# Kernel optimization log

Hardware: AMD Instinct MI355X
Metric: run time of the kernel (lower is better)

## Reference

```python
import jax, jax.numpy as jnp
import numpy as np

# dims
B = 4096; BEGIN = 0; END = 2048; N_OBJ = 64; D_OBJ = 32
PI_IN = 31; PI_H = 256; EMB = 256; H = 4; HD = 64; OTH_IN = 256; OTH_H = 256; OTH_OUT = 256

def _lin_init(k, fan_in, fan_out):
    b = np.sqrt(6.0 / (fan_in + fan_out))
    return jax.random.uniform(k, (fan_in, fan_out), jnp.float32, -b, b)

def setup_inputs() -> dict:
    key = jax.random.key(0)
    ks = jax.random.split(key, 8)
    obs = jax.random.normal(ks[0], (B, BEGIN + (END - BEGIN) + OTH_IN), jnp.float32)
    inp = {
        "obs": obs,
        # others encoder MLP: 256 -> 256 -> 256
        "oW1": _lin_init(ks[1], OTH_IN, OTH_H), "ob1": jnp.zeros((OTH_H,), jnp.float32),
        "oW2": _lin_init(ks[2], OTH_H, OTH_OUT), "ob2": jnp.zeros((OTH_OUT,), jnp.float32),
        # per-object pi MLP: 31 -> 256 -> 256 -> 256
        "pW1": _lin_init(ks[3], PI_IN, PI_H), "pb1": jnp.zeros((PI_H,), jnp.float32),
        "pW2": _lin_init(ks[4], PI_H, PI_H), "pb2": jnp.zeros((PI_H,), jnp.float32),
        "pW3": _lin_init(ks[5], PI_H, EMB), "pb3": jnp.zeros((EMB,), jnp.float32),
        # attention projections
        "Wq": _lin_init(ks[6], OTH_OUT, H * HD), "bq": jnp.zeros((H * HD,), jnp.float32),
        # per-head K/V projections (MultiHeadProj): [H, HD, HD], stored as x @ W per head
        "Wk": jax.random.uniform(jax.random.fold_in(key, 10), (H, HD, HD), jnp.float32, -np.sqrt(6.0/(2*HD)), np.sqrt(6.0/(2*HD))),
        "bk": jnp.zeros((H, HD), jnp.float32),
        "Wv": jax.random.uniform(jax.random.fold_in(key, 11), (H, HD, HD), jnp.float32, -np.sqrt(6.0/(2*HD)), np.sqrt(6.0/(2*HD))),
        "bv": jnp.zeros((H, HD), jnp.float32),
    }
    return inp

def reference(obs, oW1, ob1, oW2, ob2, pW1, pb1, pW2, pb2, pW3, pb3, Wq, bq, Wk, bk, Wv, bv):
    # split obs
    objs = obs[:, BEGIN:END].reshape(-1, N_OBJ, D_OBJ)
    others = jnp.concatenate([obs[:, :BEGIN], obs[:, END:]], axis=1)
    # others encoder
    others_e = jax.nn.relu(others @ oW1 + ob1) @ oW2 + ob2           # [B, 256]
    # mask + per-object MLP
    mask = objs[:, :, -1]                                            # [B, N]
    feats = objs[:, :, :-1]                                          # [B, N, 31]
    h = jax.nn.relu(feats @ pW1 + pb1)
    h = jax.nn.relu(h @ pW2 + pb2)
    emb = (h @ pW3 + pb3) * mask[:, :, None]                         # [B, N, EMB]
    # attention
    q = (others_e @ Wq + bq).reshape(-1, H, 1, HD)                   # [B, H, 1, HD]
    e = emb.reshape(-1, N_OBJ, H, HD)                                # [B, N, H, HD]
    key = jnp.einsum('bnhd,hde->bnhe', e, Wk) + bk                   # per-head linear
    val = (jnp.einsum('bnhd,hde->bnhe', e, Wv) + bv) * mask[:, :, None, None]
    logits = jnp.einsum('bhqd,bnhd->bhqn', q, key) / np.sqrt(EMB)    # [B, H, 1, N]
    logits = jnp.where(mask[:, None, None, :] == 0, -1e9, logits)
    attn = jax.nn.softmax(logits, axis=-1)
    out_emb = jnp.einsum('bhqn,bnhd->bhqd', attn, val).reshape(-1, EMB)
    return jnp.concatenate([others_e, out_emb], axis=1)             # [B, 512]
```

## Files before the change

kernel.cpp:

```cpp
#include <hip/hip_runtime.h>

#define BATCH      4096
#define OBS_COLS   2304
#define OTH_OFF    2048
#define EMB        256
#define OUTC       512

#define QK_BYTES   (4096u * 256u * 4u)
#define QB_BYTES   (4096u * 4u * 4u)

typedef __bf16 bf16x8 __attribute__((ext_vector_type(8)));
typedef __bf16 bf16x4 __attribute__((ext_vector_type(4)));
typedef float  f32x16 __attribute__((ext_vector_type(16)));

#define S_PW1  0
#define S_PW2  2
#define S_PW3  18
#define N_SLICE 34

__device__ __forceinline__ int shx(int row, int col) {
    return (row << 8) + ((((col >> 3) ^ (row & 31)) << 3) | (col & 7));
}

__global__ __launch_bounds__(512, 2) void k_oth(
    const float* __restrict__ obs,
    const float* __restrict__ oW1, const float* __restrict__ ob1,
    const float* __restrict__ oW2, const float* __restrict__ ob2,
    const float* __restrict__ Wq,  const float* __restrict__ bq,
    const float* __restrict__ Wk,  const float* __restrict__ bk,
    const float* __restrict__ pW1, const float* __restrict__ pW2,
    const float* __restrict__ pW3,
    float* __restrict__ out, float* __restrict__ qkg,
    float* __restrict__ qbg, __bf16* __restrict__ wp)
{
    __shared__ __align__(16) __bf16 s_a[32 * 256];
    __shared__ __align__(16) __bf16 s_h[32 * 256];
    __shared__ __align__(16) __bf16 s_q[32 * 256];
    __shared__ float s_qb[32 * 4];

    const int t  = threadIdx.x;
    const int b0 = blockIdx.x * 32;
    const int wv = t >> 6, lane = t & 63;
    const int lm = lane & 31, lh = lane >> 5;
    const int ct = wv;

    if (blockIdx.x < N_SLICE) {
        const int s = blockIdx.x;
        int kt; const float* W; int isW1 = 0;
        if      (s < S_PW2) { kt = s;         W = pW1; isW1 = 1; }
        else if (s < S_PW3) { kt = s - S_PW2; W = pW2; }
        else                { kt = s - S_PW3; W = pW3; }
        const int kbase = kt * 16 + lh * 8;
        const int n     = (t >> 6) * 32 + lm;
        bf16x8 v;
        #pragma unroll
        for (int j = 0; j < 8; ++j) {
            const int k = kbase + j;
            const float f = (isW1 && k >= 31) ? 0.0f : W[k * 256 + n];
            v[j] = (__bf16)f;
        }
        ((bf16x8*)wp)[(size_t)s * 512 + t] = v;
    }

    #pragma unroll
    for (int i = 0; i < 2; ++i) {
        const int c = i * 512 + t;
        const int row = c >> 5, seg = c & 31;
        const float* src = obs + (size_t)(b0 + row) * OBS_COLS + OTH_OFF + seg * 8;
        const float4 v0 = ((const float4*)src)[0];
        const float4 v1 = ((const float4*)src)[1];
        bf16x8 o;
        o[0]=(__bf16)v0.x; o[1]=(__bf16)v0.y; o[2]=(__bf16)v0.z; o[3]=(__bf16)v0.w;
        o[4]=(__bf16)v1.x; o[5]=(__bf16)v1.y; o[6]=(__bf16)v1.z; o[7]=(__bf16)v1.w;
        *(bf16x8*)&s_a[shx(row, seg * 8)] = o;
    }
    if (t < 128) s_qb[t] = 0.0f;
    __syncthreads();

    f32x16 acc;
    f32x16 vzero;
    #pragma unroll
    for (int i = 0; i < 16; ++i) vzero[i] = 0.0f;

    {
        const float* Wl = oW1 + (size_t)(lh * 8) * 256 + ct * 32 + lm;
        acc = vzero;
        float f[8];
        #pragma unroll
        for (int j = 0; j < 8; ++j) f[j] = Wl[j * 256];
        #pragma unroll 4
        for (int kt = 0; kt < 16; ++kt) {
            float fn[8];
            const int kn = (kt + 1) & 15;
            #pragma unroll
            for (int j = 0; j < 8; ++j) fn[j] = Wl[(kn * 16 + j) * 256];
            bf16x8 b;
            #pragma unroll
            for (int j = 0; j < 8; ++j) b[j] = (__bf16)f[j];
            const bf16x8 a = *(const bf16x8*)&s_a[shx(lm, kt * 16 + lh * 8)];
            acc = __builtin_amdgcn_mfma_f32_32x32x16_bf16(b, a, acc, 0, 0, 0);
            #pragma unroll
            for (int j = 0; j < 8; ++j) f[j] = fn[j];
        }
        const float* bias = &ob1[ct * 32 + 4 * lh];
        #pragma unroll
        for (int g = 0; g < 4; ++g) {
            bf16x4 v;
            #pragma unroll
            for (int q = 0; q < 4; ++q)
                v[q] = (__bf16)fmaxf(acc[g * 4 + q] + bias[8 * g + q], 0.0f);
            *(bf16x4*)&s_h[(lm << 8) + ((((ct << 2) + g) ^ lm) << 3) + 4 * lh] = v;
        }
    }
    __syncthreads();

    {
        const float* Wl = oW2 + (size_t)(lh * 8) * 256 + ct * 32 + lm;
        acc = vzero;
        float f[8];
        #pragma unroll
        for (int j = 0; j < 8; ++j) f[j] = Wl[j * 256];
        #pragma unroll 4
        for (int kt = 0; kt < 16; ++kt) {
            float fn[8];
            const int kn = (kt + 1) & 15;
            #pragma unroll
            for (int j = 0; j < 8; ++j) fn[j] = Wl[(kn * 16 + j) * 256];
            bf16x8 b;
            #pragma unroll
            for (int j = 0; j < 8; ++j) b[j] = (__bf16)f[j];
            const bf16x8 a = *(const bf16x8*)&s_h[shx(lm, kt * 16 + lh * 8)];
            acc = __builtin_amdgcn_mfma_f32_32x32x16_bf16(b, a, acc, 0, 0, 0);
            #pragma unroll
            for (int j = 0; j < 8; ++j) f[j] = fn[j];
        }
        const float* bias = &ob2[ct * 32 + 4 * lh];
        float* dstg = &out[(size_t)(b0 + lm) * OUTC + ct * 32 + 4 * lh];
        #pragma unroll
        for (int g = 0; g < 4; ++g) {
            float4 fv; bf16x4 v;
            float* fp = &fv.x;
            #pragma unroll
            for (int q = 0; q < 4; ++q) {
                const float f2 = acc[g * 4 + q] + bias[8 * g + q];
                fp[q] = f2; v[q] = (__bf16)f2;
            }
            *(float4*)&dstg[8 * g] = fv;
            *(bf16x4*)&s_a[(lm << 8) + ((((ct << 2) + g) ^ lm) << 3) + 4 * lh] = v;
        }
    }
    __syncthreads();

    {
        const float* Wl = Wq + (size_t)(lh * 8) * 256 + ct * 32 + lm;
        acc = vzero;
        float f[8];
        #pragma unroll
        for (int j = 0; j < 8; ++j) f[j] = Wl[j * 256];
        #pragma unroll 4
        for (int kt = 0; kt < 16; ++kt) {
            float fn[8];
            const int kn = (kt + 1) & 15;
            #pragma unroll
            for (int j = 0; j < 8; ++j) fn[j] = Wl[(kn * 16 + j) * 256];
            bf16x8 b;
            #pragma unroll
            for (int j = 0; j < 8; ++j) b[j] = (__bf16)f[j];
            const bf16x8 a = *(const bf16x8*)&s_a[shx(lm, kt * 16 + lh * 8)];
            acc = __builtin_amdgcn_mfma_f32_32x32x16_bf16(b, a, acc, 0, 0, 0);
            #pragma unroll
            for (int j = 0; j < 8; ++j) f[j] = fn[j];
        }
        const int hh = ct >> 1;
        const float* bias = &bq[ct * 32 + 4 * lh];
        const float* bkp  = &bk[ct * 32 + 4 * lh];
        float part = 0.0f;
        #pragma unroll
        for (int g = 0; g < 4; ++g) {
            bf16x4 v;
            #pragma unroll
            for (int q = 0; q < 4; ++q) {
                const float f2 = acc[g * 4 + q] + bias[8 * g + q];
                part += f2 * bkp[8 * g + q];
                v[q] = (__bf16)f2;
            }
            *(bf16x4*)&s_q[(lm << 8) + ((((ct << 2) + g) ^ lm) << 3) + 4 * lh] = v;
        }
        part += __shfl_xor(part, 32, 64);
        if (lane < 32) atomicAdd(&s_qb[lm * 4 + hh], part);
    }
    __syncthreads();

    if (t < 128) qbg[(size_t)(b0 + (t >> 2)) * 4 + (t & 3)] = s_qb[t];

    {
        const int h = wv >> 1, c2 = wv & 1;
        acc = vzero;
        #pragma unroll
        for (int kt = 0; kt < 4; ++kt) {
            const float* wk = Wk + ((size_t)(h * 64 + c2 * 32 + lm) * 64 + kt * 16 + lh * 8);
            const float4 w0 = *(const float4*)wk;
            const float4 w1 = *(const float4*)(wk + 4);
            bf16x8 b;
            b[0]=(__bf16)w0.x; b[1]=(__bf16)w0.y; b[2]=(__bf16)w0.z; b[3]=(__bf16)w0.w;
            b[4]=(__bf16)w1.x; b[5]=(__bf16)w1.y; b[6]=(__bf16)w1.z; b[7]=(__bf16)w1.w;
            const bf16x8 a = *(const bf16x8*)&s_q[shx(lm, h * 64 + kt * 16 + lh * 8)];
            acc = __builtin_amdgcn_mfma_f32_32x32x16_bf16(b, a, acc, 0, 0, 0);
        }
        float* dstg = &qkg[(size_t)(b0 + lm) * 256 + h * 64 + c2 * 32 + 4 * lh];
        #pragma unroll
        for (int g = 0; g < 4; ++g) {
            float4 fv;
            float* fp = &fv.x;
            #pragma unroll
            for (int q = 0; q < 4; ++q) fp[q] = acc[g * 4 + q];
            *(float4*)&dstg[8 * g] = fv;
        }
    }
}

__global__ __launch_bounds__(256, 4) void k_obj(
    const float* __restrict__ obs,  const __bf16* __restrict__ wp,
    const float* __restrict__ pb1,  const float* __restrict__ pb2,
    const float* __restrict__ pb3,  const float* __restrict__ qkg,
    const float* __restrict__ qbg,  const float* __restrict__ bv,
    const float* __restrict__ Wv,   float* __restrict__ out)
{
    __shared__ __align__(16) __bf16 s_h[64 * 256];
    __shared__ __align__(16) char s_fp[64 * 32 * 2];
    __bf16* s_f = (__bf16*)s_fp;
    float*  s_p = (float*)s_fp;
    __shared__ float s_mask[64];
    __shared__ float s_qk[4 * 64];
    __shared__ float s_am[4 * 64];
    __shared__ float s_amsum[4];
    __shared__ float s_qb[4];

    const int t  = threadIdx.x;
    const int b  = blockIdx.x;
    const int wv = t >> 6, lane = t & 63;
    const int lm = lane & 31, lh = lane >> 5;
    const int ct0 = wv * 2;
    const int row0 = lm;
    const int row1 = lm + 32;

    bf16x8 b1[2][2];
    {
        const bf16x8* Bg = (const bf16x8*)wp + S_PW1 * 512;
        #pragma unroll
        for (int kt = 0; kt < 2; ++kt)
            #pragma unroll
            for (int c = 0; c < 2; ++c)
                b1[kt][c] = Bg[(kt * 8 + ct0 + c) * 64 + lane];
    }

    {
        const int row = t >> 2, q4 = t & 3;
        const float* src = obs + (size_t)b * OBS_COLS + row * 32 + q4 * 8;
        const float4 v0 = ((const float4*)src)[0];
        const float4 v1 = ((const float4*)src)[1];
        bf16x8 o;
        o[0]=(__bf16)v0.x; o[1]=(__bf16)v0.y; o[2]=(__bf16)v0.z; o[3]=(__bf16)v0.w;
        o[4]=(__bf16)v1.x; o[5]=(__bf16)v1.y; o[6]=(__bf16)v1.z; o[7]=(__bf16)v1.w;
        *(bf16x8*)&s_f[row * 32 + q4 * 8] = o;
        if (q4 == 3) s_mask[row] = v1.w;
    }
    if (t < 64) ((float4*)s_qk)[t] = ((const float4*)(qkg + (size_t)b * 256))[t];
    if (t >= 64 && t < 68) s_qb[t - 64] = qbg[(size_t)b * 4 + (t - 64)];
    __syncthreads();

    f32x16 acc[2][2];
    f32x16 vzero;
    #pragma unroll
    for (int i = 0; i < 16; ++i) vzero[i] = 0.0f;

    {
        #pragma unroll
        for (int r = 0; r < 2; ++r)
            #pragma unroll
            for (int c = 0; c < 2; ++c) acc[r][c] = vzero;
        #pragma unroll
        for (int kt = 0; kt < 2; ++kt) {
            const bf16x8 a0 = *(const bf16x8*)&s_f[row0 * 32 + kt * 16 + lh * 8];
            const bf16x8 a1 = *(const bf16x8*)&s_f[row1 * 32 + kt * 16 + lh * 8];
            acc[0][0] = __builtin_amdgcn_mfma_f32_32x32x16_bf16(b1[kt][0], a0, acc[0][0], 0, 0, 0);
            acc[0][1] = __builtin_amdgcn_mfma_f32_32x32x16_bf16(b1[kt][1], a0, acc[0][1], 0, 0, 0);
            acc[1][0] = __builtin_amdgcn_mfma_f32_32x32x16_bf16(b1[kt][0], a1, acc[1][0], 0, 0, 0);
            acc[1][1] = __builtin_amdgcn_mfma_f32_32x32x16_bf16(b1[kt][1], a1, acc[1][1], 0, 0, 0);
        }
        #pragma unroll
        for (int r = 0; r < 2; ++r) {
            const int row = r ? row1 : row0;
            #pragma unroll
            for (int c = 0; c < 2; ++c) {
                const float* bias = &pb1[(ct0 + c) * 32 + 4 * lh];
                #pragma unroll
                for (int g = 0; g < 4; ++g) {
                    bf16x4 v;
                    #pragma unroll
                    for (int q = 0; q < 4; ++q)
                        v[q] = (__bf16)fmaxf(acc[r][c][g * 4 + q] + bias[8 * g + q], 0.0f);
                    *(bf16x4*)&s_h[(row << 8) + (((((ct0 + c) << 2) + g) ^ lm) << 3) + 4 * lh] = v;
                }
            }
        }
    }
    __syncthreads();

    {
        const bf16x8* Bg = (const bf16x8*)wp + S_PW2 * 512;
        #pragma unroll
        for (int r = 0; r < 2; ++r)
            #pragma unroll
            for (int c = 0; c < 2; ++c) acc[r][c] = vzero;
        bf16x8 bc0 = Bg[(ct0 + 0) * 64 + lane];
        bf16x8 bc1 = Bg[(ct0 + 1) * 64 + lane];
        #pragma unroll 4
        for (int kt = 0; kt < 16; ++kt) {
            const int kn = (kt + 1) & 15;
            const bf16x8 bn0 = Bg[(kn * 8 + ct0 + 0) * 64 + lane];
            const bf16x8 bn1 = Bg[(kn * 8 + ct0 + 1) * 64 + lane];
            const bf16x8 a0 = *(const bf16x8*)&s_h[(row0 << 8) + (((2 * kt + lh) ^ lm) << 3)];
            const bf16x8 a1 = *(const bf16x8*)&s_h[(row1 << 8) + (((2 * kt + lh) ^ lm) << 3)];
            acc[0][0] = __builtin_amdgcn_mfma_f32_32x32x16_bf16(bc0, a0, acc[0][0], 0, 0, 0);
            acc[0][1] = __builtin_amdgcn_mfma_f32_32x32x16_bf16(bc1, a0, acc[0][1], 0, 0, 0);
            acc[1][0] = __builtin_amdgcn_mfma_f32_32x32x16_bf16(bc0, a1, acc[1][0], 0, 0, 0);
            acc[1][1] = __builtin_amdgcn_mfma_f32_32x32x16_bf16(bc1, a1, acc[1][1], 0, 0, 0);
            bc0 = bn0; bc1 = bn1;
        }
        __syncthreads();
        #pragma unroll
        for (int r = 0; r < 2; ++r) {
            const int row = r ? row1 : row0;
            #pragma unroll
            for (int c = 0; c < 2; ++c) {
                const float* bias = &pb2[(ct0 + c) * 32 + 4 * lh];
                #pragma unroll
                for (int g = 0; g < 4; ++g) {
                    bf16x4 v;
                    #pragma unroll
                    for (int q = 0; q < 4; ++q)
                        v[q] = (__bf16)fmaxf(acc[r][c][g * 4 + q] + bias[8 * g + q], 0.0f);
                    *(bf16x4*)&s_h[(row << 8) + (((((ct0 + c) << 2) + g) ^ lm) << 3) + 4 * lh] = v;
                }
            }
        }
    }
    __syncthreads();

    {
        const bf16x8* Bg = (const bf16x8*)wp + S_PW3 * 512;
        #pragma unroll
        for (int r = 0; r < 2; ++r)
            #pragma unroll
            for (int c = 0; c < 2; ++c) acc[r][c] = vzero;
        bf16x8 bc0 = Bg[(ct0 + 0) * 64 + lane];
        bf16x8 bc1 = Bg[(ct0 + 1) * 64 + lane];
        #pragma unroll 4
        for (int kt = 0; kt < 16; ++kt) {
            const int kn = (kt + 1) & 15;
            const bf16x8 bn0 = Bg[(kn * 8 + ct0 + 0) * 64 + lane];
            const bf16x8 bn1 = Bg[(kn * 8 + ct0 + 1) * 64 + lane];
            const bf16x8 a0 = *(const bf16x8*)&s_h[(row0 << 8) + (((2 * kt + lh) ^ lm) << 3)];
            const bf16x8 a1 = *(const bf16x8*)&s_h[(row1 << 8) + (((2 * kt + lh) ^ lm) << 3)];
            acc[0][0] = __builtin_amdgcn_mfma_f32_32x32x16_bf16(bc0, a0, acc[0][0], 0, 0, 0);
            acc[0][1] = __builtin_amdgcn_mfma_f32_32x32x16_bf16(bc1, a0, acc[0][1], 0, 0, 0);
            acc[1][0] = __builtin_amdgcn_mfma_f32_32x32x16_bf16(bc0, a1, acc[1][0], 0, 0, 0);
            acc[1][1] = __builtin_amdgcn_mfma_f32_32x32x16_bf16(bc1, a1, acc[1][1], 0, 0, 0);
            bc0 = bn0; bc1 = bn1;
        }
        __syncthreads();
        #pragma unroll
        for (int r = 0; r < 2; ++r) {
            const int row = r ? row1 : row0;
            const float mk = s_mask[row];
            #pragma unroll
            for (int c = 0; c < 2; ++c) {
                const float* bias = &pb3[(ct0 + c) * 32 + 4 * lh];
                #pragma unroll
                for (int g = 0; g < 4; ++g) {
                    bf16x4 v;
                    #pragma unroll
                    for (int q = 0; q < 4; ++q)
                        v[q] = (__bf16)((acc[r][c][g * 4 + q] + bias[8 * g + q]) * mk);
                    *(bf16x4*)&s_h[(row << 8) + (((((ct0 + c) << 2) + g) ^ lm) << 3) + 4 * lh] = v;
                }
            }
        }
    }
    __syncthreads();

    {
        const int h = wv;
        const float qb = s_qb[h];
        float dot = 0.0f;
        #pragma unroll
        for (int d8 = 0; d8 < 8; ++d8) {
            const bf16x8 ev = *(const bf16x8*)&s_h[(lane << 8) + ((((h << 3) + d8) ^ (lane & 31)) << 3)];
            const float* kv = &s_qk[h * 64 + d8 * 8];
            #pragma unroll
            for (int j = 0; j < 8; ++j) dot += (float)ev[j] * kv[j];
        }
        const float mk = s_mask[lane];
        float logit = (dot + qb) * 0.0625f;
        if (mk == 0.0f) logit = -1.0e9f;
        float m = logit;
        #pragma unroll
        for (int off = 32; off > 0; off >>= 1) m = fmaxf(m, __shfl_xor(m, off, 64));
        const float ex = __expf(logit - m);
        float ssum = ex;
        #pragma unroll
        for (int off = 32; off > 0; off >>= 1) ssum += __shfl_xor(ssum, off, 64);
        const float am = (ex / ssum) * mk;
        s_am[h * 64 + lane] = am;
        float ams = am;
        #pragma unroll
        for (int off = 32; off > 0; off >>= 1) ams += __shfl_xor(ams, off, 64);
        if (lane == 0) s_amsum[h] = ams;
    }
    __syncthreads();

    {
        const int h = wv, dblk = lane >> 3, j = lane & 7;
        const int blk = (h << 3) + dblk;
        float a[8];
        #pragma unroll
        for (int dd = 0; dd < 8; ++dd) a[dd] = 0.0f;
        #pragma unroll
        for (int nn = 0; nn < 8; ++nn) {
            const int n = j * 8 + nn;
            const bf16x8 ev = *(const bf16x8*)&s_h[(n << 8) + ((blk ^ (n & 31)) << 3)];
            const float amv = s_am[h * 64 + n];
            #pragma unroll
            for (int dd = 0; dd < 8; ++dd) a[dd] += amv * (float)ev[dd];
        }
        #pragma unroll
        for (int off = 1; off <= 4; off <<= 1)
            #pragma unroll
            for (int dd = 0; dd < 8; ++dd) a[dd] += __shfl_xor(a[dd], off, 64);
        const float s01 = (j & 1) ? a[1] : a[0];
        const float s23 = (j & 1) ? a[3] : a[2];
        const float s45 = (j & 1) ? a[5] : a[4];
        const float s67 = (j & 1) ? a[7] : a[6];
        const float t03 = (j & 2) ? s23 : s01;
        const float t47 = (j & 2) ? s67 : s45;
        const float val = (j & 4) ? t47 : t03;
        s_p[h * 64 + dblk * 8 + j] = val;
    }
    __syncthreads();

    {
        const int h = wv, eblk = lane >> 3, j = lane & 7;
        const float4 p0 = *(const float4*)&s_p[h * 64 + j * 8];
        const float4 p1 = *(const float4*)&s_p[h * 64 + j * 8 + 4];
        float pd[8] = {p0.x, p0.y, p0.z, p0.w, p1.x, p1.y, p1.z, p1.w};
        float a[8];
        #pragma unroll
        for (int ee = 0; ee < 8; ++ee) a[ee] = 0.0f;
        const float* wvb = Wv + (size_t)h * 4096 + eblk * 8;
        #pragma unroll
        for (int dd = 0; dd < 8; ++dd) {
            const int d = j * 8 + dd;
            const float4 w0 = *(const float4*)&wvb[d * 64];
            const float4 w1 = *(const float4*)&wvb[d * 64 + 4];
            a[0] += pd[dd] * w0.x; a[1] += pd[dd] * w0.y;
            a[2] += pd[dd] * w0.z; a[3] += pd[dd] * w0.w;
            a[4] += pd[dd] * w1.x; a[5] += pd[dd] * w1.y;
            a[6] += pd[dd] * w1.z; a[7] += pd[dd] * w1.w;
        }
        #pragma unroll
        for (int off = 1; off <= 4; off <<= 1)
            #pragma unroll
            for (int ee = 0; ee < 8; ++ee) a[ee] += __shfl_xor(a[ee], off, 64);
        const float s01 = (j & 1) ? a[1] : a[0];
        const float s23 = (j & 1) ? a[3] : a[2];
        const float s45 = (j & 1) ? a[5] : a[4];
        const float s67 = (j & 1) ? a[7] : a[6];
        const float t03 = (j & 2) ? s23 : s01;
        const float t47 = (j & 2) ? s67 : s45;
        float val = (j & 4) ? t47 : t03;
        val += s_amsum[h] * bv[h * 64 + lane];
        out[(size_t)b * OUTC + EMB + h * 64 + lane] = val;
    }
}

extern "C" void kernel_launch(void* const* d_in, const int* in_sizes, int n_in,
                              void* d_out, int out_size, void* d_ws, size_t ws_size,
                              hipStream_t stream)
{
    const float* obs = (const float*)d_in[0];
    const float* oW1 = (const float*)d_in[1];
    const float* ob1 = (const float*)d_in[2];
    const float* oW2 = (const float*)d_in[3];
    const float* ob2 = (const float*)d_in[4];
    const float* pW1 = (const float*)d_in[5];
    const float* pb1 = (const float*)d_in[6];
    const float* pW2 = (const float*)d_in[7];
    const float* pb2 = (const float*)d_in[8];
    const float* pW3 = (const float*)d_in[9];
    const float* pb3 = (const float*)d_in[10];
    const float* Wq  = (const float*)d_in[11];
    const float* bq  = (const float*)d_in[12];
    const float* Wk  = (const float*)d_in[13];
    const float* bk  = (const float*)d_in[14];
    const float* Wv  = (const float*)d_in[15];
    const float* bv  = (const float*)d_in[16];
    float*  out = (float*)d_out;
    float*  qkg = (float*)d_ws;
    float*  qbg = (float*)((char*)d_ws + QK_BYTES);
    __bf16* wp  = (__bf16*)((char*)d_ws + QK_BYTES + QB_BYTES);

    k_oth<<<BATCH / 32, 512, 0, stream>>>(obs, oW1, ob1, oW2, ob2, Wq, bq,
                                          Wk, bk, pW1, pW2, pW3,
                                          out, qkg, qbg, wp);
    k_obj<<<BATCH, 256, 0, stream>>>(obs, wp, pb1, pb2, pb3, qkg, qbg,
                                     bv, Wv, out);
}
```

Baseline: 240.7 us.

## Process two batch rows per k_obj block with 512 threads and deeper weight prefetch

```diff
diff --git a/kernel.cpp b/kernel.cpp
--- a/kernel.cpp
+++ b/kernel.cpp
@@ -219,30 +219,30 @@
     }
 }
 
-__global__ __launch_bounds__(256, 4) void k_obj(
+__global__ __launch_bounds__(512, 4) void k_obj(
     const float* __restrict__ obs,  const __bf16* __restrict__ wp,
     const float* __restrict__ pb1,  const float* __restrict__ pb2,
     const float* __restrict__ pb3,  const float* __restrict__ qkg,
     const float* __restrict__ qbg,  const float* __restrict__ bv,
     const float* __restrict__ Wv,   float* __restrict__ out)
 {
-    __shared__ __align__(16) __bf16 s_h[64 * 256];
-    __shared__ __align__(16) char s_fp[64 * 32 * 2];
+    __shared__ __align__(16) __bf16 s_h[128 * 256];
+    __shared__ __align__(16) char s_fp[128 * 40 * 2];
     __bf16* s_f = (__bf16*)s_fp;
     float*  s_p = (float*)s_fp;
-    __shared__ float s_mask[64];
-    __shared__ float s_qk[4 * 64];
-    __shared__ float s_am[4 * 64];
-    __shared__ float s_amsum[4];
-    __shared__ float s_qb[4];
+    __shared__ float s_mask[128];
+    __shared__ float s_qk[8 * 64];
+    __shared__ float s_am[8 * 64];
+    __shared__ float s_amsum[8];
 
     const int t  = threadIdx.x;
-    const int b  = blockIdx.x;
+    const int b0 = blockIdx.x * 2;
     const int wv = t >> 6, lane = t & 63;
     const int lm = lane & 31, lh = lane >> 5;
-    const int ct0 = wv * 2;
-    const int row0 = lm;
-    const int row1 = lm + 32;
+    const int rtp = wv & 1;
+    const int ct0 = (wv >> 1) * 2;
+    const int row0 = rtp * 64 + lm;
+    const int row1 = row0 + 32;
 
     bf16x8 b1[2][2];
     {
@@ -256,17 +256,17 @@
 
     {
         const int row = t >> 2, q4 = t & 3;
-        const float* src = obs + (size_t)b * OBS_COLS + row * 32 + q4 * 8;
+        const float* src = obs + (size_t)(b0 + (row >> 6)) * OBS_COLS
+                               + (row & 63) * 32 + q4 * 8;
         const float4 v0 = ((const float4*)src)[0];
         const float4 v1 = ((const float4*)src)[1];
         bf16x8 o;
         o[0]=(__bf16)v0.x; o[1]=(__bf16)v0.y; o[2]=(__bf16)v0.z; o[3]=(__bf16)v0.w;
         o[4]=(__bf16)v1.x; o[5]=(__bf16)v1.y; o[6]=(__bf16)v1.z; o[7]=(__bf16)v1.w;
-        *(bf16x8*)&s_f[row * 32 + q4 * 8] = o;
+        *(bf16x8*)&s_f[row * 40 + q4 * 8] = o;
         if (q4 == 3) s_mask[row] = v1.w;
     }
-    if (t < 64) ((float4*)s_qk)[t] = ((const float4*)(qkg + (size_t)b * 256))[t];
-    if (t >= 64 && t < 68) s_qb[t - 64] = qbg[(size_t)b * 4 + (t - 64)];
+    if (t < 128) ((float4*)s_qk)[t] = ((const float4*)(qkg + (size_t)b0 * 256))[t];
     __syncthreads();
 
     f32x16 acc[2][2];
@@ -281,8 +281,8 @@
             for (int c = 0; c < 2; ++c) acc[r][c] = vzero;
         #pragma unroll
         for (int kt = 0; kt < 2; ++kt) {
-            const bf16x8 a0 = *(const bf16x8*)&s_f[row0 * 32 + kt * 16 + lh * 8];
-            const bf16x8 a1 = *(const bf16x8*)&s_f[row1 * 32 + kt * 16 + lh * 8];
+            const bf16x8 a0 = *(const bf16x8*)&s_f[row0 * 40 + kt * 16 + lh * 8];
+            const bf16x8 a1 = *(const bf16x8*)&s_f[row1 * 40 + kt * 16 + lh * 8];
             acc[0][0] = __builtin_amdgcn_mfma_f32_32x32x16_bf16(b1[kt][0], a0, acc[0][0], 0, 0, 0);
             acc[0][1] = __builtin_amdgcn_mfma_f32_32x32x16_bf16(b1[kt][1], a0, acc[0][1], 0, 0, 0);
             acc[1][0] = __builtin_amdgcn_mfma_f32_32x32x16_bf16(b1[kt][0], a1, acc[1][0], 0, 0, 0);
@@ -313,20 +313,26 @@
         for (int r = 0; r < 2; ++r)
             #pragma unroll
             for (int c = 0; c < 2; ++c) acc[r][c] = vzero;
-        bf16x8 bc0 = Bg[(ct0 + 0) * 64 + lane];
-        bf16x8 bc1 = Bg[(ct0 + 1) * 64 + lane];
-        #pragma unroll 4
+        bf16x8 bb[4][2];
+        #pragma unroll
+        for (int i = 0; i < 4; ++i) {
+            bb[i][0] = Bg[(i * 8 + ct0 + 0) * 64 + lane];
+            bb[i][1] = Bg[(i * 8 + ct0 + 1) * 64 + lane];
+        }
+        #pragma unroll
         for (int kt = 0; kt < 16; ++kt) {
-            const int kn = (kt + 1) & 15;
-            const bf16x8 bn0 = Bg[(kn * 8 + ct0 + 0) * 64 + lane];
-            const bf16x8 bn1 = Bg[(kn * 8 + ct0 + 1) * 64 + lane];
+            bf16x8 bl0, bl1;
+            if (kt < 12) {
+                bl0 = Bg[((kt + 4) * 8 + ct0 + 0) * 64 + lane];
+                bl1 = Bg[((kt + 4) * 8 + ct0 + 1) * 64 + lane];
+            }
             const bf16x8 a0 = *(const bf16x8*)&s_h[(row0 << 8) + (((2 * kt + lh) ^ lm) << 3)];
             const bf16x8 a1 = *(const bf16x8*)&s_h[(row1 << 8) + (((2 * kt + lh) ^ lm) << 3)];
-            acc[0][0] = __builtin_amdgcn_mfma_f32_32x32x16_bf16(bc0, a0, acc[0][0], 0, 0, 0);
-            acc[0][1] = __builtin_amdgcn_mfma_f32_32x32x16_bf16(bc1, a0, acc[0][1], 0, 0, 0);
-            acc[1][0] = __builtin_amdgcn_mfma_f32_32x32x16_bf16(bc0, a1, acc[1][0], 0, 0, 0);
-            acc[1][1] = __builtin_amdgcn_mfma_f32_32x32x16_bf16(bc1, a1, acc[1][1], 0, 0, 0);
-            bc0 = bn0; bc1 = bn1;
+            acc[0][0] = __builtin_amdgcn_mfma_f32_32x32x16_bf16(bb[kt & 3][0], a0, acc[0][0], 0, 0, 0);
+            acc[0][1] = __builtin_amdgcn_mfma_f32_32x32x16_bf16(bb[kt & 3][1], a0, acc[0][1], 0, 0, 0);
+            acc[1][0] = __builtin_amdgcn_mfma_f32_32x32x16_bf16(bb[kt & 3][0], a1, acc[1][0], 0, 0, 0);
+            acc[1][1] = __builtin_amdgcn_mfma_f32_32x32x16_bf16(bb[kt & 3][1], a1, acc[1][1], 0, 0, 0);
+            if (kt < 12) { bb[kt & 3][0] = bl0; bb[kt & 3][1] = bl1; }
         }
         __syncthreads();
         #pragma unroll
@@ -354,20 +360,26 @@
         for (int r = 0; r < 2; ++r)
             #pragma unroll
             for (int c = 0; c < 2; ++c) acc[r][c] = vzero;
-        bf16x8 bc0 = Bg[(ct0 + 0) * 64 + lane];
-        bf16x8 bc1 = Bg[(ct0 + 1) * 64 + lane];
-        #pragma unroll 4
+        bf16x8 bb[4][2];
+        #pragma unroll
+        for (int i = 0; i < 4; ++i) {
+            bb[i][0] = Bg[(i * 8 + ct0 + 0) * 64 + lane];
+            bb[i][1] = Bg[(i * 8 + ct0 + 1) * 64 + lane];
+        }
+        #pragma unroll
         for (int kt = 0; kt < 16; ++kt) {
-            const int kn = (kt + 1) & 15;
-            const bf16x8 bn0 = Bg[(kn * 8 + ct0 + 0) * 64 + lane];
-            const bf16x8 bn1 = Bg[(kn * 8 + ct0 + 1) * 64 + lane];
+            bf16x8 bl0, bl1;
+            if (kt < 12) {
+                bl0 = Bg[((kt + 4) * 8 + ct0 + 0) * 64 + lane];
+                bl1 = Bg[((kt + 4) * 8 + ct0 + 1) * 64 + lane];
+            }
             const bf16x8 a0 = *(const bf16x8*)&s_h[(row0 << 8) + (((2 * kt + lh) ^ lm) << 3)];
             const bf16x8 a1 = *(const bf16x8*)&s_h[(row1 << 8) + (((2 * kt + lh) ^ lm) << 3)];
-            acc[0][0] = __builtin_amdgcn_mfma_f32_32x32x16_bf16(bc0, a0, acc[0][0], 0, 0, 0);
-            acc[0][1] = __builtin_amdgcn_mfma_f32_32x32x16_bf16(bc1, a0, acc[0][1], 0, 0, 0);
-            acc[1][0] = __builtin_amdgcn_mfma_f32_32x32x16_bf16(bc0, a1, acc[1][0], 0, 0, 0);
-            acc[1][1] = __builtin_amdgcn_mfma_f32_32x32x16_bf16(bc1, a1, acc[1][1], 0, 0, 0);
-            bc0 = bn0; bc1 = bn1;
+            acc[0][0] = __builtin_amdgcn_mfma_f32_32x32x16_bf16(bb[kt & 3][0], a0, acc[0][0], 0, 0, 0);
+            acc[0][1] = __builtin_amdgcn_mfma_f32_32x32x16_bf16(bb[kt & 3][1], a0, acc[0][1], 0, 0, 0);
+            acc[1][0] = __builtin_amdgcn_mfma_f32_32x32x16_bf16(bb[kt & 3][0], a1, acc[1][0], 0, 0, 0);
+            acc[1][1] = __builtin_amdgcn_mfma_f32_32x32x16_bf16(bb[kt & 3][1], a1, acc[1][1], 0, 0, 0);
+            if (kt < 12) { bb[kt & 3][0] = bl0; bb[kt & 3][1] = bl1; }
         }
         __syncthreads();
         #pragma unroll
@@ -391,17 +403,18 @@
     __syncthreads();
 
     {
-        const int h = wv;
-        const float qb = s_qb[h];
+        const int r = wv >> 2, h = wv & 3;
+        const float qb = qbg[(size_t)(b0 + r) * 4 + h];
+        const int erow = r * 64 + lane;
         float dot = 0.0f;
         #pragma unroll
         for (int d8 = 0; d8 < 8; ++d8) {
-            const bf16x8 ev = *(const bf16x8*)&s_h[(lane << 8) + ((((h << 3) + d8) ^ (lane & 31)) << 3)];
-            const float* kv = &s_qk[h * 64 + d8 * 8];
+            const bf16x8 ev = *(const bf16x8*)&s_h[(erow << 8) + ((((h << 3) + d8) ^ (erow & 31)) << 3)];
+            const float* kv = &s_qk[(r * 4 + h) * 64 + d8 * 8];
             #pragma unroll
             for (int j = 0; j < 8; ++j) dot += (float)ev[j] * kv[j];
         }
-        const float mk = s_mask[lane];
+        const float mk = s_mask[erow];
         float logit = (dot + qb) * 0.0625f;
         if (mk == 0.0f) logit = -1.0e9f;
         float m = logit;
@@ -412,16 +425,16 @@
         #pragma unroll
         for (int off = 32; off > 0; off >>= 1) ssum += __shfl_xor(ssum, off, 64);
         const float am = (ex / ssum) * mk;
-        s_am[h * 64 + lane] = am;
+        s_am[(r * 4 + h) * 64 + lane] = am;
         float ams = am;
         #pragma unroll
         for (int off = 32; off > 0; off >>= 1) ams += __shfl_xor(ams, off, 64);
-        if (lane == 0) s_amsum[h] = ams;
-    }
-    __syncthreads();
-
-    {
-        const int h = wv, dblk = lane >> 3, j = lane & 7;
+        if (lane == 0) s_amsum[r * 4 + h] = ams;
+    }
+    __syncthreads();
+
+    {
+        const int r = wv >> 2, h = wv & 3, dblk = lane >> 3, j = lane & 7;
         const int blk = (h << 3) + dblk;
         float a[8];
         #pragma unroll
@@ -429,8 +442,9 @@
         #pragma unroll
         for (int nn = 0; nn < 8; ++nn) {
             const int n = j * 8 + nn;
-            const bf16x8 ev = *(const bf16x8*)&s_h[(n << 8) + ((blk ^ (n & 31)) << 3)];
-            const float amv = s_am[h * 64 + n];
+            const int row = r * 64 + n;
+            const bf16x8 ev = *(const bf16x8*)&s_h[(row << 8) + ((blk ^ (row & 31)) << 3)];
+            const float amv = s_am[(r * 4 + h) * 64 + n];
             #pragma unroll
             for (int dd = 0; dd < 8; ++dd) a[dd] += amv * (float)ev[dd];
         }
@@ -445,14 +459,14 @@
         const float t03 = (j & 2) ? s23 : s01;
         const float t47 = (j & 2) ? s67 : s45;
         const float val = (j & 4) ? t47 : t03;
-        s_p[h * 64 + dblk * 8 + j] = val;
-    }
-    __syncthreads();
-
-    {
-        const int h = wv, eblk = lane >> 3, j = lane & 7;
-        const float4 p0 = *(const float4*)&s_p[h * 64 + j * 8];
-        const float4 p1 = *(const float4*)&s_p[h * 64 + j * 8 + 4];
+        s_p[(r * 4 + h) * 64 + dblk * 8 + j] = val;
+    }
+    __syncthreads();
+
+    {
+        const int r = wv >> 2, h = wv & 3, eblk = lane >> 3, j = lane & 7;
+        const float4 p0 = *(const float4*)&s_p[(r * 4 + h) * 64 + j * 8];
+        const float4 p1 = *(const float4*)&s_p[(r * 4 + h) * 64 + j * 8 + 4];
         float pd[8] = {p0.x, p0.y, p0.z, p0.w, p1.x, p1.y, p1.z, p1.w};
         float a[8];
         #pragma unroll
@@ -479,8 +493,8 @@
         const float t03 = (j & 2) ? s23 : s01;
         const float t47 = (j & 2) ? s67 : s45;
         float val = (j & 4) ? t47 : t03;
-        val += s_amsum[h] * bv[h * 64 + lane];
-        out[(size_t)b * OUTC + EMB + h * 64 + lane] = val;
+        val += s_amsum[r * 4 + h] * bv[h * 64 + lane];
+        out[(size_t)(b0 + r) * OUTC + EMB + h * 64 + lane] = val;
     }
 }
 
@@ -513,6 +527,6 @@
     k_oth<<<BATCH / 32, 512, 0, stream>>>(obs, oW1, ob1, oW2, ob2, Wq, bq,
                                           Wk, bk, pW1, pW2, pW3,
                                           out, qkg, qbg, wp);
-    k_obj<<<BATCH, 256, 0, stream>>>(obs, wp, pb1, pb2, pb3, qkg, qbg,
-                                     bv, Wv, out);
+    k_obj<<<BATCH / 2, 512, 0, stream>>>(obs, wp, pb1, pb2, pb3, qkg, qbg,
+                                         bv, Wv, out);
 }
```

Measured after the change: 295.1 us. 22.6% more time.
